# Kernel optimization log

Hardware: AMD Instinct MI355X
Metric: run time of the kernel (lower is better)

## Reference

```python
import jax, jax.numpy as jnp
import numpy as np
from jax import lax


def setup_inputs() -> dict:
    key = jax.random.key(0)
    k1, k2, k3, k4 = jax.random.split(key, 4)
    N, D, B, R, EF = 100000, 256, 64, 32, 32
    storage = jax.random.normal(k1, (N, D), dtype=jnp.float32)
    query = jax.random.normal(k2, (B, D), dtype=jnp.float32)
    graph = jax.random.randint(k3, (N, R), 0, N, dtype=jnp.int32)      # fixed-degree NSW adjacency
    initial = jax.random.randint(k4, (B, EF), 0, N, dtype=jnp.int32)   # random entry points (entry())
    return {"query": query, "storage": storage, "graph": graph,
            "initial": initial, "k": 10, "ef_search": EF}


def reference(query, storage, graph, initial, k, ef_search):
    """Batched greedy best-first NSW search (ef_search fixed expansion steps)."""
    N = storage.shape[0]
    INF = jnp.float32(1e30)

    def sqdist(q, ids):
        diff = storage[ids] - q            # [R, D] gather
        return jnp.sum(diff * diff, axis=-1)

    def search_one(q, init):
        cd = sqdist(q, init)                               # candidate distances [EF]
        visited = jnp.zeros((N,), jnp.bool_).at[init].set(True)
        expanded = jnp.zeros((N,), jnp.bool_)

        def step(state, _):
            cid, cd, visited, expanded = state
            # pick closest unexpanded candidate
            pickd = jnp.where(expanded[cid], INF, cd)
            j = jnp.argmin(pickd)
            u = cid[j]
            expanded = expanded.at[u].set(True)
            # expand neighbors of u
            nbrs = graph[u]                                # [R]
            fresh = ~visited[nbrs]
            nd = jnp.where(fresh, sqdist(q, nbrs), INF)    # skip already-visited
            visited = visited.at[nbrs].set(True)
            # merge candidate pool, keep ef_search best
            all_ids = jnp.concatenate([cid, nbrs])
            all_d = jnp.concatenate([cd, nd])
            negd, idx = lax.top_k(-all_d, ef_search)
            return (all_ids[idx], -negd, visited, expanded), None

        (cid, cd, _, _), _ = lax.scan(step, (init, cd, visited, expanded),
                                      None, length=ef_search)
        negk, idx = lax.top_k(-cd, k)
        return cid[idx], -negk

    topk_ids, topk_dists = jax.vmap(search_one)(query, initial)
    return topk_ids, topk_dists
```

## Files before the change

kernel.cpp:

```cpp
#include <hip/hip_runtime.h>


#define DIMS   256
#define RDEG   32
#define EFPOOL 32
#define KOUT   10
#define NWORDS 3125
#define INF_D  1e30f

__global__ __launch_bounds__(64, 1) void nsw_wave_kernel(
    const float* __restrict__ query,
    const float* __restrict__ storage,
    const int*   __restrict__ graph,
    const int*   __restrict__ initial,
    float*       __restrict__ out,
    int B)
{
    __shared__ unsigned int visited[NWORDS];
    __shared__ unsigned int expanded[NWORDS];
    __shared__ float sc_d[EFPOOL];
    __shared__ int   sc_id[EFPOOL];

    const int l    = threadIdx.x;
    const int b    = blockIdx.x;
    const int nb   = l & 31;
    const int half = l >> 5;

    for (int i = l; i < NWORDS; i += 64) { visited[i] = 0u; expanded[i] = 0u; }

    float4 qv[32];
    {
        const float4* qp = reinterpret_cast<const float4*>(query + (size_t)b * DIMS) + half * 32;
        #pragma unroll
        for (int j = 0; j < 32; ++j) qv[j] = qp[j];
    }

    auto halfdist = [&](int id) -> float {
        const float4* sp = reinterpret_cast<const float4*>(storage + (size_t)id * DIMS) + half * 32;
        float4 r[32];
        #pragma unroll
        for (int j = 0; j < 32; ++j) r[j] = sp[j];
        float a0 = 0.f, a1 = 0.f, a2 = 0.f, a3 = 0.f;
        #pragma unroll
        for (int j = 0; j < 32; ++j) {
            float d0 = r[j].x - qv[j].x; a0 = fmaf(d0, d0, a0);
            float d1 = r[j].y - qv[j].y; a1 = fmaf(d1, d1, a1);
            float d2 = r[j].z - qv[j].z; a2 = fmaf(d2, d2, a2);
            float d3 = r[j].w - qv[j].w; a3 = fmaf(d3, d3, a3);
        }
        return (a0 + a1) + (a2 + a3);
    };

    int pool_id = initial[b * EFPOOL + nb];
    if (l < 32) atomicOr(&visited[pool_id >> 5], 1u << (pool_id & 31));
    float pool_d;
    {
        float part = halfdist(pool_id);
        pool_d = part + __shfl_xor(part, 32, 64);
    }

    for (int step = 0; step < EFPOOL; ++step) {
        unsigned ew = expanded[pool_id >> 5];
        bool ex = (ew >> (pool_id & 31)) & 1u;
        float pd = ex ? INF_D : pool_d;
        int   ix = nb;
        #pragma unroll
        for (int m = 16; m >= 1; m >>= 1) {
            float od = __shfl_xor(pd, m, 64);
            int   oi = __shfl_xor(ix, m, 64);
            if (od < pd || (od == pd && oi < ix)) { pd = od; ix = oi; }
        }
        int jx = __builtin_amdgcn_readfirstlane(ix);
        int u  = __shfl(pool_id, jx, 64);
        if (l == 0) atomicOr(&expanded[u >> 5], 1u << (u & 31));

        int nbid = graph[(size_t)u * RDEG + nb];
        unsigned vw = visited[nbid >> 5];
        bool fresh = !((vw >> (nbid & 31)) & 1u);
        if (l < 32 && fresh) atomicOr(&visited[nbid >> 5], 1u << (nbid & 31));

        float part = fresh ? halfdist(nbid) : 0.f;
        float nd = part + __shfl_xor(part, 32, 64);
        if (!fresh) nd = INF_D;

        float ed  = half ? nd   : pool_d;
        int   eid = half ? nbid : pool_id;
        unsigned long long key =
            ((unsigned long long)__float_as_uint(ed) << 6) | (unsigned)l;
        int rank = 0;
        #pragma unroll
        for (int j = 0; j < 64; ++j) {
            unsigned long long kj = __shfl(key, j, 64);
            rank += (kj < key) ? 1 : 0;
        }
        if (rank < EFPOOL) { sc_d[rank] = ed; sc_id[rank] = eid; }
        pool_d  = sc_d[nb];
        pool_id = sc_id[nb];
    }

    if (l < KOUT) {
        out[b * KOUT + l]            = (float)pool_id;
        out[B * KOUT + b * KOUT + l] = pool_d;
    }
}

extern "C" void kernel_launch(void* const* d_in, const int* in_sizes, int n_in,
                              void* d_out, int out_size, void* d_ws, size_t ws_size,
                              hipStream_t stream) {
    const float* query   = (const float*)d_in[0];
    const float* storage = (const float*)d_in[1];
    const int*   graph   = (const int*)d_in[2];
    const int*   initial = (const int*)d_in[3];
    float* out = (float*)d_out;

    const int B = in_sizes[0] / DIMS;

    nsw_wave_kernel<<<B, 64, 0, stream>>>(query, storage, graph, initial, out, B);
}
```

Before: 281.4 us.

## Restructure NSW step: issue storage loads early, pick next node from sorted pool

The next node to expand is now chosen right after the merge, as the first unexpanded slot of the rank-sorted pool found with a ballot. This drops the separate shuffle argmin. Each step issues the graph and storage row loads before the visited-bit check, so memory latency overlaps the bookkeeping, and distances are computed unconditionally before masking. The query moves from registers to LDS, and the rank count reads keys from LDS instead of 64 shuffles. In exchange, rows for already-visited neighbors are now fetched too, and each step adds extra LDS traffic.

New measurement: 235.0 us. -16.5%, faster.

```diff
diff --git a/kernel.cpp b/kernel.cpp
--- a/kernel.cpp
+++ b/kernel.cpp
@@ -18,6 +18,8 @@
 {
     __shared__ unsigned int visited[NWORDS];
     __shared__ unsigned int expanded[NWORDS];
+    __shared__ float4 qsh[DIMS / 4];
+    __shared__ unsigned long long keys[64];
     __shared__ float sc_d[EFPOOL];
     __shared__ int   sc_id[EFPOOL];
 
@@ -28,74 +30,78 @@
 
     for (int i = l; i < NWORDS; i += 64) { visited[i] = 0u; expanded[i] = 0u; }
 
-    float4 qv[32];
-    {
-        const float4* qp = reinterpret_cast<const float4*>(query + (size_t)b * DIMS) + half * 32;
-        #pragma unroll
-        for (int j = 0; j < 32; ++j) qv[j] = qp[j];
-    }
+    qsh[l] = reinterpret_cast<const float4*>(query + (size_t)b * DIMS)[l];
 
-    auto halfdist = [&](int id) -> float {
-        const float4* sp = reinterpret_cast<const float4*>(storage + (size_t)id * DIMS) + half * 32;
-        float4 r[32];
-        #pragma unroll
-        for (int j = 0; j < 32; ++j) r[j] = sp[j];
-        float a0 = 0.f, a1 = 0.f, a2 = 0.f, a3 = 0.f;
-        #pragma unroll
-        for (int j = 0; j < 32; ++j) {
-            float d0 = r[j].x - qv[j].x; a0 = fmaf(d0, d0, a0);
-            float d1 = r[j].y - qv[j].y; a1 = fmaf(d1, d1, a1);
-            float d2 = r[j].z - qv[j].z; a2 = fmaf(d2, d2, a2);
-            float d3 = r[j].w - qv[j].w; a3 = fmaf(d3, d3, a3);
-        }
-        return (a0 + a1) + (a2 + a3);
-    };
+    float pool_d  = INF_D;
+    int   pool_id = 0;
+    int   u;
 
-    int pool_id = initial[b * EFPOOL + nb];
-    if (l < 32) atomicOr(&visited[pool_id >> 5], 1u << (pool_id & 31));
-    float pool_d;
-    {
-        float part = halfdist(pool_id);
-        pool_d = part + __shfl_xor(part, 32, 64);
-    }
-
-    for (int step = 0; step < EFPOOL; ++step) {
-        unsigned ew = expanded[pool_id >> 5];
-        bool ex = (ew >> (pool_id & 31)) & 1u;
-        float pd = ex ? INF_D : pool_d;
-        int   ix = nb;
-        #pragma unroll
-        for (int m = 16; m >= 1; m >>= 1) {
-            float od = __shfl_xor(pd, m, 64);
-            int   oi = __shfl_xor(ix, m, 64);
-            if (od < pd || (od == pd && oi < ix)) { pd = od; ix = oi; }
-        }
-        int jx = __builtin_amdgcn_readfirstlane(ix);
-        int u  = __shfl(pool_id, jx, 64);
-        if (l == 0) atomicOr(&expanded[u >> 5], 1u << (u & 31));
-
-        int nbid = graph[(size_t)u * RDEG + nb];
-        unsigned vw = visited[nbid >> 5];
-        bool fresh = !((vw >> (nbid & 31)) & 1u);
-        if (l < 32 && fresh) atomicOr(&visited[nbid >> 5], 1u << (nbid & 31));
-
-        float part = fresh ? halfdist(nbid) : 0.f;
-        float nd = part + __shfl_xor(part, 32, 64);
-        if (!fresh) nd = INF_D;
-
+    auto merge_pick = [&](float nd, int nbid) {
         float ed  = half ? nd   : pool_d;
         int   eid = half ? nbid : pool_id;
         unsigned long long key =
             ((unsigned long long)__float_as_uint(ed) << 6) | (unsigned)l;
+        keys[l] = key;
         int rank = 0;
         #pragma unroll
-        for (int j = 0; j < 64; ++j) {
-            unsigned long long kj = __shfl(key, j, 64);
-            rank += (kj < key) ? 1 : 0;
-        }
+        for (int j = 0; j < 64; ++j)
+            rank += (keys[j] < key) ? 1 : 0;
         if (rank < EFPOOL) { sc_d[rank] = ed; sc_id[rank] = eid; }
         pool_d  = sc_d[nb];
         pool_id = sc_id[nb];
+        bool unexp = !((expanded[pool_id >> 5] >> (pool_id & 31)) & 1u);
+        unsigned long long m = __ballot(unexp && (l < 32));
+        int slot = (m == 0ull) ? 0 : (__ffsll((unsigned long long)m) - 1);
+        u = sc_id[slot];
+        if (l == 0) expanded[u >> 5] |= (1u << (u & 31));
+    };
+
+    {
+        int nbid = initial[b * EFPOOL + nb];
+        const float4* sp = reinterpret_cast<const float4*>(storage + (size_t)nbid * DIMS) + half * 32;
+        float4 r[32];
+        #pragma unroll
+        for (int j = 0; j < 32; ++j) r[j] = sp[j];
+        if (l < 32) atomicOr(&visited[nbid >> 5], 1u << (nbid & 31));
+        float a0 = 0.f, a1 = 0.f, a2 = 0.f, a3 = 0.f;
+        #pragma unroll
+        for (int j = 0; j < 32; ++j) {
+            float4 q = qsh[half * 32 + j];
+            float d0 = r[j].x - q.x; a0 = fmaf(d0, d0, a0);
+            float d1 = r[j].y - q.y; a1 = fmaf(d1, d1, a1);
+            float d2 = r[j].z - q.z; a2 = fmaf(d2, d2, a2);
+            float d3 = r[j].w - q.w; a3 = fmaf(d3, d3, a3);
+        }
+        float part = (a0 + a1) + (a2 + a3);
+        float nd = part + __shfl_xor(part, 32, 64);
+        merge_pick(nd, nbid);
+    }
+
+    for (int step = 0; step < EFPOOL; ++step) {
+        int nbid = graph[(size_t)u * RDEG + nb];
+        const float4* sp = reinterpret_cast<const float4*>(storage + (size_t)nbid * DIMS) + half * 32;
+        float4 r[32];
+        #pragma unroll
+        for (int j = 0; j < 32; ++j) r[j] = sp[j];
+
+        unsigned vw = visited[nbid >> 5];
+        bool fresh = !((vw >> (nbid & 31)) & 1u);
+        if ((l < 32) && fresh) atomicOr(&visited[nbid >> 5], 1u << (nbid & 31));
+
+        float a0 = 0.f, a1 = 0.f, a2 = 0.f, a3 = 0.f;
+        #pragma unroll
+        for (int j = 0; j < 32; ++j) {
+            float4 q = qsh[half * 32 + j];
+            float d0 = r[j].x - q.x; a0 = fmaf(d0, d0, a0);
+            float d1 = r[j].y - q.y; a1 = fmaf(d1, d1, a1);
+            float d2 = r[j].z - q.z; a2 = fmaf(d2, d2, a2);
+            float d3 = r[j].w - q.w; a3 = fmaf(d3, d3, a3);
+        }
+        float part = (a0 + a1) + (a2 + a3);
+        float d = part + __shfl_xor(part, 32, 64);
+        float nd = fresh ? d : INF_D;
+
+        merge_pick(nd, nbid);
     }
 
     if (l < KOUT) {
```
